# Performance work log

Measured on AMD Instinct MI355X. Metric: run time of the kernel, lower is better.

The kernel has to match this reference:

```python
import jax, jax.numpy as jnp
import numpy as np


def _lstm_layer(x, W_ih, W_hh, b):
    # x: [B, T, D_in]; W_ih: [4H, D_in]; W_hh: [4H, H]; b: [4H]
    H = W_hh.shape[1]
    # Precompute input-to-hidden GEMM for all timesteps (batched, efficient).
    xg = jnp.einsum('bti,gi->btg', x, W_ih) + b  # [B, T, 4H]
    B = x.shape[0]
    h0 = jnp.zeros((B, H), dtype=x.dtype)
    c0 = jnp.zeros((B, H), dtype=x.dtype)

    def step(carry, xg_t):
        h, c = carry
        g = xg_t + h @ W_hh.T                     # [B, 4H]
        i, f, gg, o = jnp.split(g, 4, axis=-1)    # torch LSTMCell gate order
        i = jax.nn.sigmoid(i)
        f = jax.nn.sigmoid(f)
        gg = jnp.tanh(gg)
        o = jax.nn.sigmoid(o)
        c = f * c + i * gg
        h = o * jnp.tanh(c)
        return (h, c), h

    (h_last, c_last), hs = jax.lax.scan(step, (h0, c0), jnp.swapaxes(xg, 0, 1))
    return jnp.swapaxes(hs, 0, 1), h_last, c_last  # [B,T,H], [B,H], [B,H]


def setup_inputs() -> dict:
    key = jax.random.key(0)
    ks = jax.random.split(key, 6)
    B, T, D, H = 64, 2048, 256, 256
    s = 0.05  # small init scale for numerical stability over 2048 steps
    return {
        'x': jax.random.normal(ks[0], (B, T, D), dtype=jnp.float32),
        'W_ih0': jax.random.normal(ks[1], (4 * H, D), dtype=jnp.float32) * s,
        'W_hh0': jax.random.normal(ks[2], (4 * H, H), dtype=jnp.float32) * s,
        'b0': jnp.zeros((4 * H,), dtype=jnp.float32),
        'W_ih1': jax.random.normal(ks[3], (4 * H, H), dtype=jnp.float32) * s,
        'W_hh1': jax.random.normal(ks[4], (4 * H, H), dtype=jnp.float32) * s,
        'b1': jnp.zeros((4 * H,), dtype=jnp.float32),
    }


def reference(x, W_ih0, W_hh0, b0, W_ih1, W_hh1, b1):
    # 2-layer unidirectional LSTM, matching RNNBase(mode='LSTM') forward:
    # returns (h_seq_of_last_layer [B,T,H], (h_last, c_last) of last layer)
    h1, _, _ = _lstm_layer(x, W_ih0, W_hh0, b0)
    h2, h_last, c_last = _lstm_layer(h1, W_ih1, W_hh1, b1)
    return h2, h_last, c_last
```

## Files before the change

kernel.cpp:

```cpp
#include <hip/hip_runtime.h>
#include <hip/hip_bf16.h>


typedef unsigned short u16;
typedef unsigned int   u32;

typedef __attribute__((ext_vector_type(8))) _Float16       half8;
typedef __attribute__((ext_vector_type(2))) _Float16       half2_t;
typedef __attribute__((ext_vector_type(8))) unsigned short ushort8;
typedef __attribute__((ext_vector_type(4))) float          f32x4;

#define B_  64
#define T_  2048
#define D_  256
#define H_  256
#define G_  1024

#define NRG 46
#define NLD 18
static_assert(NRG + NLD == 64, "k-split coverage");

__device__ __forceinline__ u16 f2h(float f) {
    union { _Float16 h; u16 b; } v; v.h = (_Float16)f; return v.b;
}
__device__ __forceinline__ float dot2(u32 w, u32 hv, float acc) {
#if __has_builtin(__builtin_amdgcn_fdot2)
    union { u32 u; half2_t h; } a, b;
    a.u = w; b.u = hv;
    return __builtin_amdgcn_fdot2(a.h, b.h, acc, false);
#else
    union { u32 u; _Float16 h[2]; } a, b;
    a.u = w; b.u = hv;
    acc += (float)a.h[0] * (float)b.h[0];
    acc += (float)a.h[1] * (float)b.h[1];
    return acc;
#endif
}
__device__ __forceinline__ float sigm(float x) {
    return 1.0f / (1.0f + __expf(-x));
}
__device__ __forceinline__ float tanh_(float x) {
    float e = __expf(-2.0f * fabsf(x));
    float r = (1.0f - e) / (1.0f + e);
    return x < 0.0f ? -r : r;
}

__global__ __launch_bounds__(256) void pack_whh(
    const float* __restrict__ W0, const float* __restrict__ W1,
    uint4* __restrict__ P0, uint4* __restrict__ P1)
{
    const int k2 = blockIdx.x;
    const int j  = threadIdx.x;
    const float* W = blockIdx.y ? W1 : W0;
    uint4*       P = blockIdx.y ? P1 : P0;
    uint4 v;
    u32* vp = &v.x;
#pragma unroll
    for (int g = 0; g < 4; ++g) {
        float2 w = *(const float2*)(W + (size_t)(g * 256 + j) * 256 + 2 * k2);
        vp[g] = (u32)f2h(w.x) | ((u32)f2h(w.y) << 16);
    }
    P[(size_t)k2 * 256 + j] = v;
}

__global__ __launch_bounds__(256) void pack_wih(
    const float* __restrict__ W0, const float* __restrict__ W1,
    u16* __restrict__ O0, u16* __restrict__ O1)
{
    const float* W = blockIdx.y ? W1 : W0;
    u16*         O = blockIdx.y ? O1 : O0;
    size_t i = (size_t)blockIdx.x * 256 + threadIdx.x;
    float4 v = ((const float4*)W)[i];
    u32 lo = (u32)f2h(v.x) | ((u32)f2h(v.y) << 16);
    u32 hi = (u32)f2h(v.z) | ((u32)f2h(v.w) << 16);
    uint2 u; u.x = lo; u.y = hi;
    ((uint2*)O)[i] = u;
}

template<int AHALF>
__global__ __launch_bounds__(256) void gemm_xg(
    const void* __restrict__ Av, const u16* __restrict__ Bh,
    u16* __restrict__ out, int tclog2, int Tstride, int t0)
{
    __shared__ __align__(16) u16 As[64][264];
    const int tid    = threadIdx.x;
    const int m0     = blockIdx.x * 64;
    const int tcmask = (1 << tclog2) - 1;

    if (AHALF) {
        const u16* Ah = (const u16*)Av;
#pragma unroll
        for (int it = 0; it < 8; ++it) {
            int idx = it * 256 + tid;
            int row = idx >> 5;
            int c8  = idx & 31;
            int m   = m0 + row;
            size_t grow = (size_t)(m >> tclog2) * Tstride + t0 + (m & tcmask);
            ushort8 v = *(const ushort8*)(Ah + grow * D_ + c8 * 8);
            *(ushort8*)(&As[row][c8 * 8]) = v;
        }
    } else {
        const float* Af = (const float*)Av;
#pragma unroll
        for (int it = 0; it < 16; ++it) {
            int idx = it * 256 + tid;
            int row = idx >> 6;
            int c4  = idx & 63;
            int m   = m0 + row;
            size_t grow = (size_t)(m >> tclog2) * Tstride + t0 + (m & tcmask);
            float4 v = *(const float4*)(Af + grow * D_ + c4 * 4);
            uint2 u;
            u.x = (u32)f2h(v.x) | ((u32)f2h(v.y) << 16);
            u.y = (u32)f2h(v.z) | ((u32)f2h(v.w) << 16);
            *(uint2*)(&As[row][c4 * 4]) = u;
        }
    }
    __syncthreads();

    const int l   = tid & 63;
    const int w   = tid >> 6;
    const int rl  = l & 15;
    const int kg  = l >> 4;
    const int rr0 = kg * 4;

    for (int nb = 0; nb < 8; ++nb) {
        const int n0 = nb * 128 + w * 32;
        f32x4 zz = {0.f, 0.f, 0.f, 0.f};
        f32x4 acc[4][2];
#pragma unroll
        for (int mi = 0; mi < 4; ++mi)
#pragma unroll
            for (int ni = 0; ni < 2; ++ni) acc[mi][ni] = zz;

#pragma unroll
        for (int ks = 0; ks < 8; ++ks) {
            const int k = ks * 32 + kg * 8;
            half8 a[4], bb[2];
#pragma unroll
            for (int mi = 0; mi < 4; ++mi)
                a[mi] = *(const half8*)(&As[mi * 16 + rl][k]);
#pragma unroll
            for (int ni = 0; ni < 2; ++ni)
                bb[ni] = *(const half8*)(Bh + (size_t)(n0 + ni * 16 + rl) * D_ + k);
#pragma unroll
            for (int mi = 0; mi < 4; ++mi)
#pragma unroll
                for (int ni = 0; ni < 2; ++ni)
                    acc[mi][ni] = __builtin_amdgcn_mfma_f32_16x16x32_f16(
                        a[mi], bb[ni], acc[mi][ni], 0, 0, 0);
        }

#pragma unroll
        for (int mi = 0; mi < 4; ++mi)
#pragma unroll
            for (int ni = 0; ni < 2; ++ni) {
                f32x4 d = acc[mi][ni];
                size_t mrow = (size_t)(m0 + mi * 16 + rr0);
                int col = n0 + ni * 16 + rl;
#pragma unroll
                for (int r = 0; r < 4; ++r)
                    out[(mrow + r) * G_ + col] = f2h(d[r]);
            }
    }
}

struct ScanJob {
    const _Float16* xg;
    const uint4*    Wp;
    const float*    bias;
    float*          state;
    void*           h_out;
    float*          hc_last;
    int Tc;
    int toff;
    int TS;
    int houth;
    int first;
};

__global__ __launch_bounds__(512, 2) void lstm_scan2(ScanJob JA, ScanJob JB)
{
    const ScanJob J = (blockIdx.x >= 64) ? JB : JA;
    if (J.Tc == 0) return;
    const int b   = blockIdx.x & 63;
    const int tid = threadIdx.x;
    const int j   = tid & 255;
    const int kh  = tid >> 8;

    __shared__ __align__(16) uint4  wl[NLD][512];
    __shared__ __align__(16) u32    hf_p[128];
    __shared__ __align__(16) float4 red[256];

    const uint4* wpb = J.Wp + (size_t)(kh * 64) * 256 + j;
    uint4 wr[NRG];
#pragma unroll
    for (int p = 0; p < NRG; ++p)
        wr[p] = wpb[(size_t)p * 256];
#pragma unroll
    for (int p = 0; p < NLD; ++p)
        wl[p][tid] = wpb[(size_t)(NRG + p) * 256];

    const int Tc = J.Tc;
    const int houth = J.houth;
    float h = 0.f, c = 0.f;
    float bi = 0.f, bf_ = 0.f, bg = 0.f, bo = 0.f;
    const _Float16* xg = J.xg;
    size_t xo = (size_t)b * Tc * G_ + j;
    float nx0 = 0.f, nx1 = 0.f, nx2 = 0.f, nx3 = 0.f;
    _Float16* hfh = (_Float16*)hf_p;

    if (kh == 0) {
        if (!J.first) {
            h = J.state[b * H_ + j];
            c = J.state[B_ * H_ + b * H_ + j];
        }
        bi  = J.bias[j];
        bf_ = J.bias[256 + j];
        bg  = J.bias[512 + j];
        bo  = J.bias[768 + j];
        hfh[j] = (_Float16)h;
        nx0 = (float)xg[xo];       nx1 = (float)xg[xo + 256];
        nx2 = (float)xg[xo + 512]; nx3 = (float)xg[xo + 768];
    }
    const uint4* hv4p = ((const uint4*)hf_p) + kh * 16;
    float* hof = (float*)J.h_out;
    u16*   hoh = (u16*)J.h_out;
    size_t ho = ((size_t)b * J.TS + J.toff) * H_ + j;
    __syncthreads();

    for (int t = 0; t < Tc; ++t) {
        float a0, a1, a2, a3;
        if (kh == 0) {
            a0 = nx0 + bi; a1 = nx1 + bf_; a2 = nx2 + bg; a3 = nx3 + bo;
            if (t + 1 < Tc) xo += G_;
            nx0 = (float)xg[xo];       nx1 = (float)xg[xo + 256];
            nx2 = (float)xg[xo + 512]; nx3 = (float)xg[xo + 768];
        } else {
            a0 = a1 = a2 = a3 = 0.f;
        }

#pragma unroll
        for (int i = 0; i < 16; ++i) {
            uint4 hv4 = hv4p[i];
            const u32* hq = &hv4.x;
#pragma unroll
            for (int q = 0; q < 4; ++q) {
                const int p = 4 * i + q;
                uint4 wv;
                if (p < NRG) wv = wr[p];
                else         wv = wl[p - NRG][tid];
                u32 hv = hq[q];
                a0 = dot2(wv.x, hv, a0);
                a1 = dot2(wv.y, hv, a1);
                a2 = dot2(wv.z, hv, a2);
                a3 = dot2(wv.w, hv, a3);
            }
        }

        if (kh == 1) {
            float4 r4; r4.x = a0; r4.y = a1; r4.z = a2; r4.w = a3;
            red[j] = r4;
        }
        __syncthreads();
        if (kh == 0) {
            float4 r4 = red[j];
            a0 += r4.x; a1 += r4.y; a2 += r4.z; a3 += r4.w;
            float i_ = sigm(a0);
            float f_ = sigm(a1);
            float g_ = tanh_(a2);
            float o_ = sigm(a3);
            c = f_ * c + i_ * g_;
            float hn = o_ * tanh_(c);
            h = hn;
            hfh[j] = (_Float16)hn;
            if (houth) hoh[ho] = f2h(hn);
            else       __builtin_nontemporal_store(hn, hof + ho);
            ho += H_;
        }
        __syncthreads();
    }

    if (kh == 0) {
        J.state[b * H_ + j] = h;
        J.state[B_ * H_ + b * H_ + j] = c;
        if (J.hc_last) {
            J.hc_last[b * H_ + j] = h;
            J.hc_last[B_ * H_ + b * H_ + j] = c;
        }
    }
}

extern "C" void kernel_launch(void* const* d_in, const int* in_sizes, int n_in,
                              void* d_out, int out_size, void* d_ws, size_t ws_size,
                              hipStream_t stream)
{
    (void)in_sizes; (void)n_in; (void)out_size;

    const float* x    = (const float*)d_in[0];
    const float* Wih0 = (const float*)d_in[1];
    const float* Whh0 = (const float*)d_in[2];
    const float* b0   = (const float*)d_in[3];
    const float* Wih1 = (const float*)d_in[4];
    const float* Whh1 = (const float*)d_in[5];
    const float* b1   = (const float*)d_in[6];

    float* out   = (float*)d_out;
    float* hlast = out + (size_t)B_ * T_ * H_;

    char* ws = (char*)d_ws;
    const size_t WPB  = (size_t)128 * 256 * 16;
    const size_t WIHB = (size_t)1024 * 256 * 2;
    const size_t STB  = (size_t)2 * B_ * H_ * 4;
    uint4* Wp0    = (uint4*)(ws);
    uint4* Wp1    = (uint4*)(ws + WPB);
    u16*   Wih0h  = (u16*)(ws + 2 * WPB);
    u16*   Wih1h  = (u16*)(ws + 2 * WPB + WIHB);
    float* state0 = (float*)(ws + 2 * WPB + 2 * WIHB);
    float* state1 = (float*)(ws + 2 * WPB + 2 * WIHB + STB);
    const size_t BASE = 2 * WPB + 2 * WIHB + 2 * STB;

    int Tc = 16;
    for (int tc = 256; tc >= 16; tc >>= 1)
        if (BASE + (size_t)tc * 294912 <= ws_size) { Tc = tc; break; }
    const int nch    = T_ / Tc;
    const int tclog2 = 31 - __builtin_clz((unsigned)Tc);
    const size_t H1CB = (size_t)B_ * Tc * H_ * 2;
    const size_t XGB  = (size_t)B_ * Tc * G_ * 2;
    u16*      h1c = (u16*)(ws + BASE);
    _Float16* xgA = (_Float16*)(ws + BASE + H1CB);
    _Float16* xgB = (_Float16*)(ws + BASE + H1CB + XGB);

    pack_whh<<<dim3(128, 2), 256, 0, stream>>>(Whh0, Whh1, Wp0, Wp1);
    pack_wih<<<dim3(256, 2), 256, 0, stream>>>(Wih0, Wih1, Wih0h, Wih1h);

    const int gemmWG = (B_ * Tc) / 64;

    gemm_xg<0><<<gemmWG, 256, 0, stream>>>(x, Wih0h, (u16*)xgA, tclog2, T_, 0);

    for (int s = 0; s <= nch; ++s) {
        ScanJob JA = {}; JA.Tc = 0;
        ScanJob JB = {}; JB.Tc = 0;
        if (s < nch) {
            JA.xg = xgA;  JA.Wp = Wp0;  JA.bias = b0;  JA.state = state0;
            JA.h_out = h1c;  JA.hc_last = nullptr;
            JA.Tc = Tc;  JA.toff = 0;  JA.TS = Tc;  JA.houth = 1;
            JA.first = (s == 0);
        }
        if (s >= 1) {
            int c = s - 1;
            JB.xg = xgB;  JB.Wp = Wp1;  JB.bias = b1;  JB.state = state1;
            JB.h_out = out;  JB.hc_last = (c == nch - 1) ? hlast : nullptr;
            JB.Tc = Tc;  JB.toff = c * Tc;  JB.TS = T_;  JB.houth = 0;
            JB.first = (c == 0);
        }
        lstm_scan2<<<128, 512, 0, stream>>>(JA, JB);

        if (s + 1 < nch)
            gemm_xg<0><<<gemmWG, 256, 0, stream>>>(
                x, Wih0h, (u16*)xgA, tclog2, T_, (s + 1) * Tc);
        if (s < nch)
            gemm_xg<1><<<gemmWG, 256, 0, stream>>>(
                h1c, Wih1h, (u16*)xgB, tclog2, Tc, 0);
    }
}
```

Baseline: 3.964 ms.

## Split recurrent matvec K dimension four ways across 1024-thread blocks

Each block now has 1024 threads, and every group of 256 threads handles a quarter of the hidden-dimension reduction. Before, the split was in halves across 512 threads. Register-resident weights per thread drop from 46 to 23 uint4, with 9 per thread staged in LDS, and three partial sums are reduced through shared memory. The goal is to shorten the serial dot-product chain per timestep and add waves to hide latency. In exchange, each step does more LDS reduction traffic and synchronizes a larger block.

```diff
diff --git a/kernel.cpp b/kernel.cpp
--- a/kernel.cpp
+++ b/kernel.cpp
@@ -16,9 +16,9 @@
 #define H_  256
 #define G_  1024
 
-#define NRG 46
-#define NLD 18
-static_assert(NRG + NLD == 64, "k-split coverage");
+#define NRG 23
+#define NLD 9
+static_assert(NRG + NLD == 32, "quarter k-split coverage");
 
 __device__ __forceinline__ u16 f2h(float f) {
     union { _Float16 h; u16 b; } v; v.h = (_Float16)f; return v.b;
@@ -178,20 +178,20 @@
     int first;
 };
 
-__global__ __launch_bounds__(512, 2) void lstm_scan2(ScanJob JA, ScanJob JB)
+__global__ __launch_bounds__(1024, 4) void lstm_scan2(ScanJob JA, ScanJob JB)
 {
     const ScanJob J = (blockIdx.x >= 64) ? JB : JA;
     if (J.Tc == 0) return;
     const int b   = blockIdx.x & 63;
     const int tid = threadIdx.x;
     const int j   = tid & 255;
-    const int kh  = tid >> 8;
-
-    __shared__ __align__(16) uint4  wl[NLD][512];
+    const int kq  = tid >> 8;
+
+    __shared__ __align__(16) uint4  wl[NLD][1024];
     __shared__ __align__(16) u32    hf_p[128];
-    __shared__ __align__(16) float4 red[256];
-
-    const uint4* wpb = J.Wp + (size_t)(kh * 64) * 256 + j;
+    __shared__ __align__(16) float4 red[3 * 256];
+
+    const uint4* wpb = J.Wp + (size_t)(kq * 32) * 256 + j;
     uint4 wr[NRG];
 #pragma unroll
     for (int p = 0; p < NRG; ++p)
@@ -209,7 +209,7 @@
     float nx0 = 0.f, nx1 = 0.f, nx2 = 0.f, nx3 = 0.f;
     _Float16* hfh = (_Float16*)hf_p;
 
-    if (kh == 0) {
+    if (kq == 0) {
         if (!J.first) {
             h = J.state[b * H_ + j];
             c = J.state[B_ * H_ + b * H_ + j];
@@ -222,7 +222,7 @@
         nx0 = (float)xg[xo];       nx1 = (float)xg[xo + 256];
         nx2 = (float)xg[xo + 512]; nx3 = (float)xg[xo + 768];
     }
-    const uint4* hv4p = ((const uint4*)hf_p) + kh * 16;
+    const uint4* hv4p = ((const uint4*)hf_p) + kq * 8;
     float* hof = (float*)J.h_out;
     u16*   hoh = (u16*)J.h_out;
     size_t ho = ((size_t)b * J.TS + J.toff) * H_ + j;
@@ -230,7 +230,7 @@
 
     for (int t = 0; t < Tc; ++t) {
         float a0, a1, a2, a3;
-        if (kh == 0) {
+        if (kq == 0) {
             a0 = nx0 + bi; a1 = nx1 + bf_; a2 = nx2 + bg; a3 = nx3 + bo;
             if (t + 1 < Tc) xo += G_;
             nx0 = (float)xg[xo];       nx1 = (float)xg[xo + 256];
@@ -240,7 +240,7 @@
         }
 
 #pragma unroll
-        for (int i = 0; i < 16; ++i) {
+        for (int i = 0; i < 8; ++i) {
             uint4 hv4 = hv4p[i];
             const u32* hq = &hv4.x;
 #pragma unroll
@@ -257,14 +257,19 @@
             }
         }
 
-        if (kh == 1) {
+        if (kq > 0) {
             float4 r4; r4.x = a0; r4.y = a1; r4.z = a2; r4.w = a3;
-            red[j] = r4;
+            red[(kq - 1) * 256 + j] = r4;
         }
         __syncthreads();
-        if (kh == 0) {
-            float4 r4 = red[j];
-            a0 += r4.x; a1 += r4.y; a2 += r4.z; a3 += r4.w;
+        if (kq == 0) {
+            float4 p0 = red[j];
+            float4 p1 = red[256 + j];
+            float4 p2 = red[512 + j];
+            a0 += p0.x + p1.x + p2.x;
+            a1 += p0.y + p1.y + p2.y;
+            a2 += p0.z + p1.z + p2.z;
+            a3 += p0.w + p1.w + p2.w;
             float i_ = sigm(a0);
             float f_ = sigm(a1);
             float g_ = tanh_(a2);
@@ -280,7 +285,7 @@
         __syncthreads();
     }
 
-    if (kh == 0) {
+    if (kq == 0) {
         J.state[b * H_ + j] = h;
         J.state[B_ * H_ + b * H_ + j] = c;
         if (J.hc_last) {
@@ -353,7 +358,7 @@
             JB.Tc = Tc;  JB.toff = c * Tc;  JB.TS = T_;  JB.houth = 0;
             JB.first = (c == 0);
         }
-        lstm_scan2<<<128, 512, 0, stream>>>(JA, JB);
+        lstm_scan2<<<128, 1024, 0, stream>>>(JA, JB);
 
         if (s + 1 < nch)
             gemm_xg<0><<<gemmWG, 256, 0, stream>>>(
```

Measured after the change: 4.501 ms. +13.6%, slower.

## Split k-halves within a wavefront and reduce with permlane32 swap

Applied to the files above, without the earlier changes.

The scan kernel's two k-halves now sit in the two 32-lane halves of each wavefront instead of separate thread groups. The partial gate sums are combined with v_permlane32_swap rather than a shared-memory float4 exchange, which removes one __syncthreads per step. The hidden-state buffer becomes double-buffered by step parity. To free registers, fewer weight chunks are kept in registers and shared memory, and 16 chunks are re-streamed from global/L2 every timestep in two prefetched batches. This trades the barrier and LDS round trip for extra per-step memory traffic and redundant gate math in both halves.

```diff
diff --git a/kernel.cpp b/kernel.cpp
--- a/kernel.cpp
+++ b/kernel.cpp
@@ -16,9 +16,10 @@
 #define H_  256
 #define G_  1024
 
-#define NRG 46
-#define NLD 18
-static_assert(NRG + NLD == 64, "k-split coverage");
+#define NRG  36
+#define NLDW 12
+#define NST  16
+static_assert(NRG + NLDW + NST == 64, "k-half coverage");
 
 __device__ __forceinline__ u16 f2h(float f) {
     union { _Float16 h; u16 b; } v; v.h = (_Float16)f; return v.b;
@@ -35,6 +36,11 @@
     acc += (float)a.h[1] * (float)b.h[1];
     return acc;
 #endif
+}
+__device__ __forceinline__ float pl32_red(float x) {
+    u32 u = __float_as_uint(x), v = u;
+    asm("v_permlane32_swap_b32 %0, %1" : "+v"(u), "+v"(v));
+    return __uint_as_float(u) + __uint_as_float(v);
 }
 __device__ __forceinline__ float sigm(float x) {
     return 1.0f / (1.0f + __expf(-x));
@@ -182,14 +188,16 @@
 {
     const ScanJob J = (blockIdx.x >= 64) ? JB : JA;
     if (J.Tc == 0) return;
-    const int b   = blockIdx.x & 63;
-    const int tid = threadIdx.x;
-    const int j   = tid & 255;
-    const int kh  = tid >> 8;
-
-    __shared__ __align__(16) uint4  wl[NLD][512];
-    __shared__ __align__(16) u32    hf_p[128];
-    __shared__ __align__(16) float4 red[256];
+    const int b    = blockIdx.x & 63;
+    const int tid  = threadIdx.x;
+    const int w    = tid >> 6;
+    const int lane = tid & 63;
+    const int kh   = lane >> 5;
+    const int jl   = lane & 31;
+    const int j    = w * 32 + jl;
+
+    __shared__ __align__(16) uint4    wl[NLDW][512];
+    __shared__ __align__(16) _Float16 hf2[2][256];
 
     const uint4* wpb = J.Wp + (size_t)(kh * 64) * 256 + j;
     uint4 wr[NRG];
@@ -197,38 +205,41 @@
     for (int p = 0; p < NRG; ++p)
         wr[p] = wpb[(size_t)p * 256];
 #pragma unroll
-    for (int p = 0; p < NLD; ++p)
+    for (int p = 0; p < NLDW; ++p)
         wl[p][tid] = wpb[(size_t)(NRG + p) * 256];
-
-    const int Tc = J.Tc;
+    const uint4* wst = wpb + (size_t)(NRG + NLDW) * 256;
+
+    const int Tc    = J.Tc;
     const int houth = J.houth;
     float h = 0.f, c = 0.f;
     float bi = 0.f, bf_ = 0.f, bg = 0.f, bo = 0.f;
     const _Float16* xg = J.xg;
     size_t xo = (size_t)b * Tc * G_ + j;
     float nx0 = 0.f, nx1 = 0.f, nx2 = 0.f, nx3 = 0.f;
-    _Float16* hfh = (_Float16*)hf_p;
-
+
+    if (!J.first)
+        c = J.state[B_ * H_ + b * H_ + j];
     if (kh == 0) {
-        if (!J.first) {
-            h = J.state[b * H_ + j];
-            c = J.state[B_ * H_ + b * H_ + j];
-        }
+        if (!J.first) h = J.state[b * H_ + j];
         bi  = J.bias[j];
         bf_ = J.bias[256 + j];
         bg  = J.bias[512 + j];
         bo  = J.bias[768 + j];
-        hfh[j] = (_Float16)h;
+        hf2[0][j] = (_Float16)h;
         nx0 = (float)xg[xo];       nx1 = (float)xg[xo + 256];
         nx2 = (float)xg[xo + 512]; nx3 = (float)xg[xo + 768];
     }
-    const uint4* hv4p = ((const uint4*)hf_p) + kh * 16;
     float* hof = (float*)J.h_out;
     u16*   hoh = (u16*)J.h_out;
     size_t ho = ((size_t)b * J.TS + J.toff) * H_ + j;
     __syncthreads();
 
     for (int t = 0; t < Tc; ++t) {
+        const int par = t & 1;
+        uint4 s1[8];
+#pragma unroll
+        for (int s = 0; s < 8; ++s) s1[s] = wst[(size_t)s * 256];
+
         float a0, a1, a2, a3;
         if (kh == 0) {
             a0 = nx0 + bi; a1 = nx1 + bf_; a2 = nx2 + bg; a3 = nx3 + bo;
@@ -239,16 +250,24 @@
             a0 = a1 = a2 = a3 = 0.f;
         }
 
+        const uint4* hvp = ((const uint4*)hf2[par]) + kh * 16;
+        uint4 s2[8];
 #pragma unroll
         for (int i = 0; i < 16; ++i) {
-            uint4 hv4 = hv4p[i];
+            if (i == 9) {
+#pragma unroll
+                for (int s = 0; s < 8; ++s) s2[s] = wst[(size_t)(8 + s) * 256];
+            }
+            uint4 hv4 = hvp[i];
             const u32* hq = &hv4.x;
 #pragma unroll
             for (int q = 0; q < 4; ++q) {
                 const int p = 4 * i + q;
                 uint4 wv;
-                if (p < NRG) wv = wr[p];
-                else         wv = wl[p - NRG][tid];
+                if (p < NRG)                wv = wr[p];
+                else if (p < NRG + NLDW)    wv = wl[p - NRG][tid];
+                else if (p < NRG + NLDW + 8) wv = s1[p - NRG - NLDW];
+                else                         wv = s2[p - NRG - NLDW - 8];
                 u32 hv = hq[q];
                 a0 = dot2(wv.x, hv, a0);
                 a1 = dot2(wv.y, hv, a1);
@@ -257,22 +276,20 @@
             }
         }
 
-        if (kh == 1) {
-            float4 r4; r4.x = a0; r4.y = a1; r4.z = a2; r4.w = a3;
-            red[j] = r4;
-        }
-        __syncthreads();
+        a0 = pl32_red(a0);
+        a1 = pl32_red(a1);
+        a2 = pl32_red(a2);
+        a3 = pl32_red(a3);
+
+        float i_ = sigm(a0);
+        float f_ = sigm(a1);
+        float g_ = tanh_(a2);
+        float o_ = sigm(a3);
+        c = f_ * c + i_ * g_;
+        float hn = o_ * tanh_(c);
+        h = hn;
         if (kh == 0) {
-            float4 r4 = red[j];
-            a0 += r4.x; a1 += r4.y; a2 += r4.z; a3 += r4.w;
-            float i_ = sigm(a0);
-            float f_ = sigm(a1);
-            float g_ = tanh_(a2);
-            float o_ = sigm(a3);
-            c = f_ * c + i_ * g_;
-            float hn = o_ * tanh_(c);
-            h = hn;
-            hfh[j] = (_Float16)hn;
+            hf2[par ^ 1][j] = (_Float16)hn;
             if (houth) hoh[ho] = f2h(hn);
             else       __builtin_nontemporal_store(hn, hof + ho);
             ho += H_;
@@ -347,11 +364,11 @@
             JA.first = (s == 0);
         }
         if (s >= 1) {
-            int c = s - 1;
+            int cc = s - 1;
             JB.xg = xgB;  JB.Wp = Wp1;  JB.bias = b1;  JB.state = state1;
-            JB.h_out = out;  JB.hc_last = (c == nch - 1) ? hlast : nullptr;
-            JB.Tc = Tc;  JB.toff = c * Tc;  JB.TS = T_;  JB.houth = 0;
-            JB.first = (c == 0);
+            JB.h_out = out;  JB.hc_last = (cc == nch - 1) ? hlast : nullptr;
+            JB.Tc = Tc;  JB.toff = cc * Tc;  JB.TS = T_;  JB.houth = 0;
+            JB.first = (cc == 0);
         }
         lstm_scan2<<<128, 512, 0, stream>>>(JA, JB);
 
```

Measured after the change: 8.318 ms. 110% more time.
